# Optimization experiments

Hardware: AMD Instinct MI355X
Metric: run time of the kernel (lower is better)

The kernel has to match this reference:

```python
import jax, jax.numpy as jnp
import numpy as np

B, S, D_MODEL, D_SPACE = 4, 2048, 1024, 64
N = 512            # size of each neuron pool (all six equal)
TOTAL = 6 * N      # neuron_emb rows
K = 8              # top_k for all four attention branches
EPS = 1e-8


def topk_sparsify(w, k):
    """Top-k sparsification with renormalization via dense one-hot scatter-sum.
    w: [..., N] softmax probs -> sparse renormalized [..., N]."""
    vals, idx = jax.lax.top_k(w, k)                       # [..., k]
    n = w.shape[-1]
    one_hot = jax.nn.one_hot(idx, n, dtype=w.dtype)       # [..., k, N]
    sparse = (one_hot * vals[..., None]).sum(axis=-2)     # [..., N]
    return sparse / (sparse.sum(axis=-1, keepdims=True) + EPS)


def setup_inputs() -> dict:
    key = jax.random.key(0)
    kx, kw, ke = jax.random.split(key, 3)
    x = jax.random.normal(kx, (B, S, D_MODEL), dtype=jnp.float32)
    W_all = jax.random.normal(kw, (D_MODEL, 6 * D_SPACE), dtype=jnp.float32) * 0.02
    b_all = jnp.zeros((6 * D_SPACE,), dtype=jnp.float32)
    neuron_emb = jax.random.normal(ke, (TOTAL, D_SPACE), dtype=jnp.float32) * 0.02
    return {"x": x, "W_all": W_all, "b_all": b_all, "neuron_emb": neuron_emb}


def reference(x, W_all, b_all, neuron_emb):
    # L2-normalized neuron embeddings (cosine-sim logits)
    emb = neuron_emb / (jnp.linalg.norm(neuron_emb, axis=-1, keepdims=True) + EPS)
    # dense projection, then split into 6 heads of d_space (deterministic: no dropout)
    proj = x @ W_all + b_all                              # [B,S,6*d_space]
    h = jnp.split(proj, 6, axis=-1)
    # neuron_emb segments: fqk, fv, rqk, rv (knowledge segments unused here)
    segs = [emb[0:N], emb[0:N], emb[N:2 * N], emb[2 * N:3 * N], emb[2 * N:3 * N], emb[3 * N:4 * N]]
    weights = []
    for hi, ei in zip(h, segs):
        logits = jnp.einsum('bsd,nd->bsn', hi, ei)        # [B,S,N]
        pref = jax.nn.softmax(logits, axis=-1)
        weights.append(topk_sparsify(pref, K))
    # [6, B, S, N]: (fqk_Q, fqk_K, fv, rqk_Q, rqk_K, rv)
    return jnp.stack(weights, axis=0)
```

## Files before the change

### kernel.cpp

```cpp
#include <hip/hip_runtime.h>
#include <math.h>

#define NB 4
#define NS 2048
#define DMODEL 1024
#define DSPACE 64
#define NPOOL 512
#define NHEADS 6
#define NTOK (NB * NS)
#define PROJN (NHEADS * DSPACE)
#define EPSF 1e-8f

__global__ __launch_bounds__(256) void k_norm_emb(const float* __restrict__ emb,
                                                  float* __restrict__ embT) {
    int row  = blockIdx.x * 4 + (threadIdx.x >> 6);
    int lane = threadIdx.x & 63;
    float v  = emb[row * DSPACE + lane];
    float ss = v * v;
#pragma unroll
    for (int off = 32; off >= 1; off >>= 1) ss += __shfl_xor(ss, off, 64);
    float nrm = sqrtf(ss) + EPSF;
    embT[lane * 2048 + row] = v / nrm;
}

#define BM 64
#define BN 64
#define BK 32

__global__ __launch_bounds__(256) void k_proj(const float* __restrict__ X,
                                              const float* __restrict__ W,
                                              const float* __restrict__ bias,
                                              float* __restrict__ P) {
    __shared__ float Xt[BK * BM];
    __shared__ float Wt[BK][BN];
    const int tid = threadIdx.x;
    const int bm  = blockIdx.x * BM;
    const int bn  = blockIdx.y * BN;
    const int tm  = (tid >> 4) << 2;
    const int tn  = (tid & 15) << 2;
    const int lxm = tid >> 3;
    const int lxk = (tid & 7) << 2;
    const int lwk = tid >> 4;
    const int lwn = (tid & 15) << 2;

    const int pgA = ((((lxm)      >> 2) ^ (lxk >> 2)) << 2) + (lxm & 3);
    const int pgB = ((((lxm + 32) >> 2) ^ (lxk >> 2)) << 2) + (lxm & 3);

    float acc[4][4] = {{0.f}};
    for (int k0 = 0; k0 < DMODEL; k0 += BK) {
        float4 xa = *(const float4*)&X[(size_t)(bm + lxm) * DMODEL + k0 + lxk];
        float4 xb = *(const float4*)&X[(size_t)(bm + lxm + 32) * DMODEL + k0 + lxk];
        float4 wa = *(const float4*)&W[(size_t)(k0 + lwk) * PROJN + bn + lwn];
        float4 wb = *(const float4*)&W[(size_t)(k0 + lwk + 16) * PROJN + bn + lwn];
        __syncthreads();
        Xt[(lxk + 0) * BM + pgA] = xa.x; Xt[(lxk + 1) * BM + pgA] = xa.y;
        Xt[(lxk + 2) * BM + pgA] = xa.z; Xt[(lxk + 3) * BM + pgA] = xa.w;
        Xt[(lxk + 0) * BM + pgB] = xb.x; Xt[(lxk + 1) * BM + pgB] = xb.y;
        Xt[(lxk + 2) * BM + pgB] = xb.z; Xt[(lxk + 3) * BM + pgB] = xb.w;
        *(float4*)&Wt[lwk][lwn] = wa;
        *(float4*)&Wt[lwk + 16][lwn] = wb;
        __syncthreads();
#pragma unroll
        for (int kk = 0; kk < BK; ++kk) {
            float4 a4 = *(const float4*)&Xt[kk * BM + ((((tm >> 2) ^ (kk >> 2)) << 2))];
            float4 b4 = *(const float4*)&Wt[kk][tn];
            float av[4] = {a4.x, a4.y, a4.z, a4.w};
            float bv[4] = {b4.x, b4.y, b4.z, b4.w};
#pragma unroll
            for (int i = 0; i < 4; ++i)
#pragma unroll
                for (int j = 0; j < 4; ++j)
                    acc[i][j] = fmaf(av[i], bv[j], acc[i][j]);
        }
    }
#pragma unroll
    for (int i = 0; i < 4; ++i) {
        float o[4];
#pragma unroll
        for (int j = 0; j < 4; ++j) o[j] = acc[i][j] + bias[bn + tn + j];
        *(float4*)&P[(size_t)(bm + tm + i) * PROJN + bn + tn] = *(float4*)&o[0];
    }
}

#define CE(arr, a, b) { float _hi = fmaxf(arr[a], arr[b]); arr[b] = fminf(arr[a], arr[b]); arr[a] = _hi; }

__global__ __launch_bounds__(256, 2) void k_router(const float* __restrict__ P,
                                                   const float* __restrict__ embT,
                                                   float* __restrict__ out) {
    __shared__ float hsh[32][DSPACE];
    const int head = blockIdx.y;
    const int t0   = blockIdx.x * 32;
    const int tid  = threadIdx.x;
    const int wid  = tid >> 6;
    const int lane = tid & 63;
    const int so = (head == 2) ? 512 : (head == 3 || head == 4) ? 1024
                 : (head == 5) ? 1536 : 0;

    for (int idx = tid; idx < 512; idx += 256) {
        int t  = idx >> 4;
        int d4 = (idx & 15) << 2;
        *(float4*)&hsh[t][d4] =
            *(const float4*)&P[(size_t)(t0 + t) * PROJN + head * DSPACE + d4];
    }
    __syncthreads();

    float acc[8][8];
#pragma unroll
    for (int t = 0; t < 8; ++t)
#pragma unroll
        for (int j = 0; j < 8; ++j) acc[t][j] = 0.f;

#pragma unroll 2
    for (int d = 0; d < DSPACE; ++d) {
        const float* er = &embT[d * 2048 + so + (lane << 3)];
        float e[8];
        *(float4*)&e[0] = *(const float4*)&er[0];
        *(float4*)&e[4] = *(const float4*)&er[4];
#pragma unroll
        for (int t = 0; t < 8; ++t) {
            float hv = hsh[(wid << 3) + t][d];
#pragma unroll
            for (int j = 0; j < 8; ++j) acc[t][j] = fmaf(hv, e[j], acc[t][j]);
        }
    }

    const size_t obase = ((size_t)head * NTOK + t0 + (wid << 3)) * NPOOL;

#pragma unroll
    for (int t = 0; t < 8; ++t) {
        float l[8], s[8];
#pragma unroll
        for (int j = 0; j < 8; ++j) { l[j] = acc[t][j]; s[j] = l[j]; }

        CE(s,0,1) CE(s,2,3) CE(s,4,5) CE(s,6,7)
        CE(s,0,2) CE(s,1,3) CE(s,4,6) CE(s,5,7)
        CE(s,1,2) CE(s,5,6)
        CE(s,0,4) CE(s,1,5) CE(s,2,6) CE(s,3,7)
        CE(s,2,4) CE(s,3,5)
        CE(s,1,2) CE(s,3,4) CE(s,5,6)

#pragma unroll
        for (int off = 1; off < 64; off <<= 1) {
            float q[8];
#pragma unroll
            for (int i = 0; i < 8; ++i) q[i] = __shfl_xor(s[i], off, 64);
            float c[8];
            c[0] = fmaxf(s[0], q[7]); c[1] = fmaxf(s[1], q[6]);
            c[2] = fmaxf(s[2], q[5]); c[3] = fmaxf(s[3], q[4]);
            c[4] = fmaxf(s[4], q[3]); c[5] = fmaxf(s[5], q[2]);
            c[6] = fmaxf(s[6], q[1]); c[7] = fmaxf(s[7], q[0]);
            CE(c,0,4) CE(c,1,5) CE(c,2,6) CE(c,3,7)
            CE(c,0,2) CE(c,1,3) CE(c,4,6) CE(c,5,7)
            CE(c,0,1) CE(c,2,3) CE(c,4,5) CE(c,6,7)
#pragma unroll
            for (int i = 0; i < 8; ++i) s[i] = c[i];
        }

        const float T = s[7];
        const float m = s[0];

        float e[8]; float zp = 0.f;
#pragma unroll
        for (int j = 0; j < 8; ++j) { e[j] = __expf(l[j] - m); zp += e[j]; }
#pragma unroll
        for (int off = 32; off >= 1; off >>= 1) zp += __shfl_xor(zp, off, 64);

        unsigned gtm = 0, eqm = 0; int cgt = 0, ceq = 0;
#pragma unroll
        for (int j = 0; j < 8; ++j) {
            if (l[j] > T)       { gtm |= 1u << j; ++cgt; }
            else if (l[j] == T) { eqm |= 1u << j; ++ceq; }
        }
        int own = (ceq << 8) | cgt;
        int inc = own;
#pragma unroll
        for (int off = 1; off < 64; off <<= 1) {
            int v = __shfl_up(inc, off, 64);
            if (lane >= off) inc += v;
        }
        int tot  = __shfl(inc, 63, 64);
        int need = 8 - (tot & 0xff);
        int eqpre = (inc - own) >> 8;
        unsigned sel = gtm;
#pragma unroll
        for (int j = 0; j < 8; ++j) {
            if ((eqm >> j) & 1u) { if (eqpre < need) sel |= 1u << j; ++eqpre; }
        }

        float s8 = 0.f;
#pragma unroll
        for (int i = 0; i < 8; ++i) s8 += __expf(s[i] - m);
        float invd = 1.0f / (s8 + EPSF * zp);

        float o[8];
#pragma unroll
        for (int j = 0; j < 8; ++j)
            o[j] = ((sel >> j) & 1u) ? e[j] * invd : 0.0f;
        float4* dst = (float4*)&out[obase + (size_t)t * NPOOL + (lane << 3)];
        dst[0] = *(float4*)&o[0];
        dst[1] = *(float4*)&o[4];
    }
}

extern "C" void kernel_launch(void* const* d_in, const int* in_sizes, int n_in,
                              void* d_out, int out_size, void* d_ws, size_t ws_size,
                              hipStream_t stream) {
    const float* x   = (const float*)d_in[0];
    const float* W   = (const float*)d_in[1];
    const float* b   = (const float*)d_in[2];
    const float* emb = (const float*)d_in[3];
    float* out  = (float*)d_out;
    float* embT = (float*)d_ws;
    float* proj = embT + 64 * 2048;

    k_norm_emb<<<dim3(512), dim3(256), 0, stream>>>(emb, embT);
    dim3 g2(NTOK / BM, PROJN / BN);
    k_proj<<<g2, dim3(256), 0, stream>>>(x, W, b, proj);
    dim3 g3(NTOK / 32, NHEADS);
    k_router<<<g3, dim3(256), 0, stream>>>(proj, embT, out);
}
```

Before: 184.1 us.

## Split-K projection GEMM with larger 8x8 microtiles and vectorized router loads

Retiles the projection GEMM to 256x64 block tiles with 8x8 per-thread microtiles. It splits the K dimension across a grid z dimension, sized by available workspace, and prefetches the next K slab into registers while computing. The router kernel sums the split-K partial slabs when staging its tokens, reads the staged activations as float4, and drops a wavefront reduction used only for the epsilon term by switching to a lane-local sum. The costs are extra partial-sum memory traffic, a dependence on workspace size, and a small numerical change in the epsilon denominator.

```diff
diff --git a/kernel.cpp b/kernel.cpp
--- a/kernel.cpp
+++ b/kernel.cpp
@@ -23,62 +23,91 @@
     embT[lane * 2048 + row] = v / nrm;
 }
 
-#define BM 64
-#define BN 64
-#define BK 32
-
-__global__ __launch_bounds__(256) void k_proj(const float* __restrict__ X,
-                                              const float* __restrict__ W,
-                                              const float* __restrict__ bias,
-                                              float* __restrict__ P) {
-    __shared__ float Xt[BK * BM];
-    __shared__ float Wt[BK][BN];
+__global__ __launch_bounds__(256, 3) void k_proj(const float* __restrict__ X,
+                                                 const float* __restrict__ W,
+                                                 const float* __restrict__ bias,
+                                                 float* __restrict__ P, int KS) {
+    __shared__ float Xt[16 * 256];
+    __shared__ float Wt[16 * 64];
     const int tid = threadIdx.x;
-    const int bm  = blockIdx.x * BM;
-    const int bn  = blockIdx.y * BN;
-    const int tm  = (tid >> 4) << 2;
-    const int tn  = (tid & 15) << 2;
-    const int lxm = tid >> 3;
-    const int lxk = (tid & 7) << 2;
-    const int lwk = tid >> 4;
-    const int lwn = (tid & 15) << 2;
-
-    const int pgA = ((((lxm)      >> 2) ^ (lxk >> 2)) << 2) + (lxm & 3);
-    const int pgB = ((((lxm + 32) >> 2) ^ (lxk >> 2)) << 2) + (lxm & 3);
-
-    float acc[4][4] = {{0.f}};
-    for (int k0 = 0; k0 < DMODEL; k0 += BK) {
-        float4 xa = *(const float4*)&X[(size_t)(bm + lxm) * DMODEL + k0 + lxk];
-        float4 xb = *(const float4*)&X[(size_t)(bm + lxm + 32) * DMODEL + k0 + lxk];
-        float4 wa = *(const float4*)&W[(size_t)(k0 + lwk) * PROJN + bn + lwn];
-        float4 wb = *(const float4*)&W[(size_t)(k0 + lwk + 16) * PROJN + bn + lwn];
+    const int bm  = blockIdx.x * 256;
+    const int bn  = blockIdx.y * 64;
+    const int z   = blockIdx.z;
+    float* Pp = P + (size_t)z * NTOK * PROJN;
+
+    const int r0 = (tid >> 3) << 2;
+    const int c0 = (tid & 7) << 2;
+    const int wr = tid >> 4;
+    const int wc = (tid & 15) << 2;
+
+    const float* Xrow = X + (size_t)(bm + tid) * DMODEL;
+
+    float acc[8][8];
+#pragma unroll
+    for (int i = 0; i < 8; ++i)
+#pragma unroll
+        for (int j = 0; j < 8; ++j) acc[i][j] = 0.f;
+
+    const int nsteps = KS >> 4;
+    int k0 = z * KS;
+    float4 xr0 = *(const float4*)&Xrow[k0 + 0];
+    float4 xr1 = *(const float4*)&Xrow[k0 + 4];
+    float4 xr2 = *(const float4*)&Xrow[k0 + 8];
+    float4 xr3 = *(const float4*)&Xrow[k0 + 12];
+    float4 wrg = *(const float4*)&W[(size_t)(k0 + wr) * PROJN + bn + wc];
+
+    for (int s = 0; s < nsteps; ++s) {
         __syncthreads();
-        Xt[(lxk + 0) * BM + pgA] = xa.x; Xt[(lxk + 1) * BM + pgA] = xa.y;
-        Xt[(lxk + 2) * BM + pgA] = xa.z; Xt[(lxk + 3) * BM + pgA] = xa.w;
-        Xt[(lxk + 0) * BM + pgB] = xb.x; Xt[(lxk + 1) * BM + pgB] = xb.y;
-        Xt[(lxk + 2) * BM + pgB] = xb.z; Xt[(lxk + 3) * BM + pgB] = xb.w;
-        *(float4*)&Wt[lwk][lwn] = wa;
-        *(float4*)&Wt[lwk + 16][lwn] = wb;
+        Xt[ 0 * 256 + tid] = xr0.x; Xt[ 1 * 256 + tid] = xr0.y;
+        Xt[ 2 * 256 + tid] = xr0.z; Xt[ 3 * 256 + tid] = xr0.w;
+        Xt[ 4 * 256 + tid] = xr1.x; Xt[ 5 * 256 + tid] = xr1.y;
+        Xt[ 6 * 256 + tid] = xr1.z; Xt[ 7 * 256 + tid] = xr1.w;
+        Xt[ 8 * 256 + tid] = xr2.x; Xt[ 9 * 256 + tid] = xr2.y;
+        Xt[10 * 256 + tid] = xr2.z; Xt[11 * 256 + tid] = xr2.w;
+        Xt[12 * 256 + tid] = xr3.x; Xt[13 * 256 + tid] = xr3.y;
+        Xt[14 * 256 + tid] = xr3.z; Xt[15 * 256 + tid] = xr3.w;
+        *(float4*)&Wt[wr * 64 + wc] = wrg;
+        if (s + 1 < nsteps) {
+            int k1 = k0 + 16;
+            xr0 = *(const float4*)&Xrow[k1 + 0];
+            xr1 = *(const float4*)&Xrow[k1 + 4];
+            xr2 = *(const float4*)&Xrow[k1 + 8];
+            xr3 = *(const float4*)&Xrow[k1 + 12];
+            wrg = *(const float4*)&W[(size_t)(k1 + wr) * PROJN + bn + wc];
+        }
         __syncthreads();
 #pragma unroll
-        for (int kk = 0; kk < BK; ++kk) {
-            float4 a4 = *(const float4*)&Xt[kk * BM + ((((tm >> 2) ^ (kk >> 2)) << 2))];
-            float4 b4 = *(const float4*)&Wt[kk][tn];
-            float av[4] = {a4.x, a4.y, a4.z, a4.w};
-            float bv[4] = {b4.x, b4.y, b4.z, b4.w};
-#pragma unroll
-            for (int i = 0; i < 4; ++i)
-#pragma unroll
-                for (int j = 0; j < 4; ++j)
+        for (int kk = 0; kk < 16; ++kk) {
+            float4 a0 = *(const float4*)&Xt[kk * 256 + r0];
+            float4 a1 = *(const float4*)&Xt[kk * 256 + r0 + 128];
+            float4 b0 = *(const float4*)&Wt[kk * 64 + c0];
+            float4 b1 = *(const float4*)&Wt[kk * 64 + c0 + 32];
+            float av[8] = {a0.x, a0.y, a0.z, a0.w, a1.x, a1.y, a1.z, a1.w};
+            float bv[8] = {b0.x, b0.y, b0.z, b0.w, b1.x, b1.y, b1.z, b1.w};
+#pragma unroll
+            for (int i = 0; i < 8; ++i)
+#pragma unroll
+                for (int j = 0; j < 8; ++j)
                     acc[i][j] = fmaf(av[i], bv[j], acc[i][j]);
         }
-    }
-#pragma unroll
-    for (int i = 0; i < 4; ++i) {
-        float o[4];
-#pragma unroll
-        for (int j = 0; j < 4; ++j) o[j] = acc[i][j] + bias[bn + tn + j];
-        *(float4*)&P[(size_t)(bm + tm + i) * PROJN + bn + tn] = *(float4*)&o[0];
+        k0 += 16;
+    }
+
+#pragma unroll
+    for (int i = 0; i < 8; ++i) {
+        int row = bm + r0 + ((i < 4) ? i : 124 + i);
+        float o0[4], o1[4];
+#pragma unroll
+        for (int j = 0; j < 4; ++j) { o0[j] = acc[i][j]; o1[j] = acc[i][4 + j]; }
+        if (z == 0) {
+#pragma unroll
+            for (int j = 0; j < 4; ++j) {
+                o0[j] += bias[bn + c0 + j];
+                o1[j] += bias[bn + c0 + 32 + j];
+            }
+        }
+        *(float4*)&Pp[(size_t)row * PROJN + bn + c0]      = *(float4*)&o0[0];
+        *(float4*)&Pp[(size_t)row * PROJN + bn + c0 + 32] = *(float4*)&o1[0];
     }
 }
 
@@ -86,7 +115,7 @@
 
 __global__ __launch_bounds__(256, 2) void k_router(const float* __restrict__ P,
                                                    const float* __restrict__ embT,
-                                                   float* __restrict__ out) {
+                                                   float* __restrict__ out, int SK) {
     __shared__ float hsh[32][DSPACE];
     const int head = blockIdx.y;
     const int t0   = blockIdx.x * 32;
@@ -99,8 +128,13 @@
     for (int idx = tid; idx < 512; idx += 256) {
         int t  = idx >> 4;
         int d4 = (idx & 15) << 2;
-        *(float4*)&hsh[t][d4] =
-            *(const float4*)&P[(size_t)(t0 + t) * PROJN + head * DSPACE + d4];
+        size_t off = (size_t)(t0 + t) * PROJN + head * DSPACE + d4;
+        float4 v = *(const float4*)&P[off];
+        for (int ks = 1; ks < SK; ++ks) {
+            float4 u = *(const float4*)&P[(size_t)ks * NTOK * PROJN + off];
+            v.x += u.x; v.y += u.y; v.z += u.z; v.w += u.w;
+        }
+        *(float4*)&hsh[t][d4] = v;
     }
     __syncthreads();
 
@@ -110,17 +144,22 @@
 #pragma unroll
         for (int j = 0; j < 8; ++j) acc[t][j] = 0.f;
 
-#pragma unroll 2
-    for (int d = 0; d < DSPACE; ++d) {
-        const float* er = &embT[d * 2048 + so + (lane << 3)];
-        float e[8];
-        *(float4*)&e[0] = *(const float4*)&er[0];
-        *(float4*)&e[4] = *(const float4*)&er[4];
-#pragma unroll
-        for (int t = 0; t < 8; ++t) {
-            float hv = hsh[(wid << 3) + t][d];
-#pragma unroll
-            for (int j = 0; j < 8; ++j) acc[t][j] = fmaf(hv, e[j], acc[t][j]);
+    for (int d4 = 0; d4 < DSPACE; d4 += 4) {
+        float4 hv[8];
+#pragma unroll
+        for (int t = 0; t < 8; ++t) hv[t] = *(const float4*)&hsh[(wid << 3) + t][d4];
+#pragma unroll
+        for (int dd = 0; dd < 4; ++dd) {
+            const float* er = &embT[(d4 + dd) * 2048 + so + (lane << 3)];
+            float e[8];
+            *(float4*)&e[0] = *(const float4*)&er[0];
+            *(float4*)&e[4] = *(const float4*)&er[4];
+#pragma unroll
+            for (int t = 0; t < 8; ++t) {
+                float hvd = ((const float*)&hv[t])[dd];
+#pragma unroll
+                for (int j = 0; j < 8; ++j) acc[t][j] = fmaf(hvd, e[j], acc[t][j]);
+            }
         }
     }
 
@@ -159,11 +198,9 @@
         const float T = s[7];
         const float m = s[0];
 
-        float e[8]; float zp = 0.f;
-#pragma unroll
-        for (int j = 0; j < 8; ++j) { e[j] = __expf(l[j] - m); zp += e[j]; }
-#pragma unroll
-        for (int off = 32; off >= 1; off >>= 1) zp += __shfl_xor(zp, off, 64);
+        float e[8]; float zl = 0.f;
+#pragma unroll
+        for (int j = 0; j < 8; ++j) { e[j] = __expf(l[j] - m); zl += e[j]; }
 
         unsigned gtm = 0, eqm = 0; int cgt = 0, ceq = 0;
 #pragma unroll
@@ -190,7 +227,7 @@
         float s8 = 0.f;
 #pragma unroll
         for (int i = 0; i < 8; ++i) s8 += __expf(s[i] - m);
-        float invd = 1.0f / (s8 + EPSF * zp);
+        float invd = 1.0f / (s8 + EPSF * zl);
 
         float o[8];
 #pragma unroll
@@ -213,9 +250,15 @@
     float* embT = (float*)d_ws;
     float* proj = embT + 64 * 2048;
 
+    size_t base = (size_t)64 * 2048 * 4;
+    size_t slab = (size_t)NTOK * PROJN * 4;
+    int SK = (ws_size >= base + 4 * slab) ? 4
+           : (ws_size >= base + 2 * slab) ? 2 : 1;
+    int KS = DMODEL / SK;
+
     k_norm_emb<<<dim3(512), dim3(256), 0, stream>>>(emb, embT);
-    dim3 g2(NTOK / BM, PROJN / BN);
-    k_proj<<<g2, dim3(256), 0, stream>>>(x, W, b, proj);
+    dim3 g2(NTOK / 256, PROJN / 64, SK);
+    k_proj<<<g2, dim3(256), 0, stream>>>(x, W, b, proj, KS);
     dim3 g3(NTOK / 32, NHEADS);
-    k_router<<<g3, dim3(256), 0, stream>>>(proj, embT, out);
-}
+    k_router<<<g3, dim3(256), 0, stream>>>(proj, embT, out, SK);
+}
```

Measured after the change: 228.6 us. 1.24x slower.
